# Performance work log

Measured on AMD Instinct MI355X. Metric: run time of the kernel, lower is better.

Reference implementation:

```python
import jax, jax.numpy as jnp
import numpy as np

D_MODEL = 1024
NUM_HEADS = 16
HEAD = D_MODEL // NUM_HEADS
SCALE = float(np.sqrt(D_MODEL))  # note: sqrt(d_model), as in source
LN_EPS = 1e-5


def setup_inputs() -> dict:
    key = jax.random.key(0)
    ks = jax.random.split(key, 12)
    B, Sq, Skv = 2, 2048, 2048
    s = 0.02
    return {
        "x": jax.random.normal(ks[0], (B, Sq, D_MODEL), jnp.float32),
        "enc_output": jax.random.normal(ks[1], (B, Skv, D_MODEL), jnp.float32),
        "Wq": jax.random.normal(ks[2], (D_MODEL, D_MODEL), jnp.float32) * s,
        "bq": jnp.zeros((D_MODEL,), jnp.float32),
        "Wk": jax.random.normal(ks[3], (D_MODEL, D_MODEL), jnp.float32) * s,
        "bk": jnp.zeros((D_MODEL,), jnp.float32),
        "Wv": jax.random.normal(ks[4], (D_MODEL, D_MODEL), jnp.float32) * s,
        "bv": jnp.zeros((D_MODEL,), jnp.float32),
        "Wo": jax.random.normal(ks[5], (D_MODEL, D_MODEL), jnp.float32) * s,
        "bo": jnp.zeros((D_MODEL,), jnp.float32),
        "gamma": jnp.ones((D_MODEL,), jnp.float32),
        "beta": jnp.zeros((D_MODEL,), jnp.float32),
    }


def _split_heads(t):
    B, S, _ = t.shape
    return t.reshape(B, S, NUM_HEADS, HEAD).transpose(0, 2, 1, 3)  # [B,H,S,hd]


def reference(x, enc_output, Wq, bq, Wk, bk, Wv, bv, Wo, bo, gamma, beta):
    q = _split_heads(x @ Wq.T + bq)           # [B,H,Sq,hd]
    k = _split_heads(enc_output @ Wk.T + bk)  # [B,H,Skv,hd]
    v = _split_heads(enc_output @ Wv.T + bv)  # [B,H,Skv,hd]
    scores = jnp.einsum("bhqd,bhkd->bhqk", q, k) / SCALE
    attn_weights = jax.nn.softmax(scores, axis=-1)  # dropout p=0 -> identity
    ctx = jnp.einsum("bhqk,bhkd->bhqd", attn_weights, v)
    B, H, Sq, hd = ctx.shape
    ctx = ctx.transpose(0, 2, 1, 3).reshape(B, Sq, H * hd)
    proj = ctx @ Wo.T + bo
    y = x + proj
    mu = jnp.mean(y, axis=-1, keepdims=True)
    var = jnp.var(y, axis=-1, keepdims=True)
    out = (y - mu) * jax.lax.rsqrt(var + LN_EPS) * gamma + beta
    return out, attn_weights
```

## Files before the change

### kernel.cpp

```cpp
#include <hip/hip_runtime.h>

typedef __attribute__((ext_vector_type(4))) float f32x4;
typedef __attribute__((ext_vector_type(8))) short bf16x8;
typedef __attribute__((ext_vector_type(4))) short s16x4;
typedef __attribute__((ext_vector_type(4))) unsigned u32x4;
typedef unsigned short u16;

#define GLOAD_LDS16(g, l)                                                      \
  __builtin_amdgcn_global_load_lds(                                            \
      (__attribute__((address_space(1))) const void*)(g),                      \
      (__attribute__((address_space(3))) void*)(l), 16, 0, 0)

static __device__ __forceinline__ u16 f2b(float f) {
  unsigned u = __builtin_bit_cast(unsigned, f);
  unsigned r = (u + 0x7fffu + ((u >> 16) & 1u)) >> 16;
  return (u16)r;
}

static __device__ __forceinline__ unsigned pk2(float lo, float hi) {
  unsigned r;
  asm("v_cvt_pk_bf16_f32 %0, %1, %2" : "=v"(r) : "v"(lo), "v"(hi));
  return r;
}

static __device__ __forceinline__ f32x4 mfma16(bf16x8 a, bf16x8 b, f32x4 c) {
  return __builtin_amdgcn_mfma_f32_16x16x32_bf16(a, b, c, 0, 0, 0);
}

static __device__ __forceinline__ int fsw(int row) {
  return (row & 7) ^ ((row & 8) >> 1);
}

__global__ __launch_bounds__(256) void cvt_bf16(const float* __restrict__ in,
                                                u16* __restrict__ out, int n4) {
  int i = blockIdx.x * 256 + threadIdx.x;
  int stride = gridDim.x * 256;
  for (; i < n4; i += stride) {
    float4 v = ((const float4*)in)[i];
    s16x4 o;
    o[0] = (short)f2b(v.x);
    o[1] = (short)f2b(v.y);
    o[2] = (short)f2b(v.z);
    o[3] = (short)f2b(v.w);
    ((s16x4*)out)[i] = o;
  }
}

__global__ __launch_bounds__(256) void cvt_w4(const float* __restrict__ w0,
                                              const float* __restrict__ w1,
                                              const float* __restrict__ w2,
                                              const float* __restrict__ w3,
                                              u16* __restrict__ o0,
                                              u16* __restrict__ o1,
                                              u16* __restrict__ o2,
                                              u16* __restrict__ o3) {
  int y = blockIdx.y;
  const float* in = (y == 0) ? w0 : (y == 1) ? w1 : (y == 2) ? w2 : w3;
  u16* out = (y == 0) ? o0 : (y == 1) ? o1 : (y == 2) ? o2 : o3;
  const int n4 = 262144;
  int i = blockIdx.x * 256 + threadIdx.x;
  int stride = gridDim.x * 256;
  for (; i < n4; i += stride) {
    float4 v = ((const float4*)in)[i];
    s16x4 o;
    o[0] = (short)f2b(v.x);
    o[1] = (short)f2b(v.y);
    o[2] = (short)f2b(v.z);
    o[3] = (short)f2b(v.w);
    ((s16x4*)out)[i] = o;
  }
}

#define QSCALE 0.0450842200278f
__global__ __launch_bounds__(256) void gemm_qkv3(
    const u16* __restrict__ xb, const u16* __restrict__ eb,
    const u16* __restrict__ Wqb, const u16* __restrict__ Wkb,
    const u16* __restrict__ Wvb, const float* __restrict__ bq,
    const float* __restrict__ bk, const float* __restrict__ bv,
    u16* __restrict__ Qd, u16* __restrict__ Kd, u16* __restrict__ Vtd) {
  __shared__ __align__(16) u16 As[128 * 32];
  __shared__ __align__(16) u16 Bs[128 * 32];
  const int K = 1024;
  int z = blockIdx.z;
  const u16* A = (z == 0) ? xb : eb;
  const u16* W = (z == 0) ? Wqb : (z == 1) ? Wkb : Wvb;
  const float* bias = (z == 0) ? bq : (z == 1) ? bk : bv;

  int tid = threadIdx.x;
  int w = tid >> 6, lane = tid & 63;
  int wr = w >> 1, wc = w & 1;
  int r16 = lane & 15, c4 = lane >> 4;
  int m0 = blockIdx.y * 128, n0 = blockIdx.x * 128;
  int srow = tid >> 2;
  int scol = (tid & 3) * 8;

  f32x4 acc[4][4] = {};

  const u16* ga0 = A + (size_t)(m0 + srow) * K + scol;
  const u16* gb0 = W + (size_t)(n0 + srow) * K + scol;
  char* asb = (char*)As + w * 1024;
  char* bsb = (char*)Bs + w * 1024;

  for (int k0 = 0; k0 < K; k0 += 32) {
    GLOAD_LDS16(ga0 + k0, asb);
    GLOAD_LDS16(ga0 + 64 * K + k0, asb + 4096);
    GLOAD_LDS16(gb0 + k0, bsb);
    GLOAD_LDS16(gb0 + 64 * K + k0, bsb + 4096);
    __syncthreads();
    bf16x8 af[4], bfr[4];
#pragma unroll
    for (int i = 0; i < 4; ++i)
      af[i] = *(const bf16x8*)(As + (wr * 64 + i * 16 + r16) * 32 + c4 * 8);
#pragma unroll
    for (int j = 0; j < 4; ++j)
      bfr[j] = *(const bf16x8*)(Bs + (wc * 64 + j * 16 + r16) * 32 + c4 * 8);
#pragma unroll
    for (int i = 0; i < 4; ++i)
#pragma unroll
      for (int j = 0; j < 4; ++j) acc[i][j] = mfma16(af[i], bfr[j], acc[i][j]);
    __syncthreads();
  }

  if (z < 2) {
    float oscale = (z == 0) ? QSCALE : 1.0f;
    u16* dst = (z == 0) ? Qd : Kd;
#pragma unroll
    for (int i = 0; i < 4; ++i) {
      int m = m0 + wr * 64 + i * 16 + c4 * 4;
      int b = m >> 11, s = m & 2047;
#pragma unroll
      for (int j = 0; j < 4; ++j) {
        int n = n0 + wc * 64 + j * 16 + r16;
        int h = n >> 6, d = n & 63;
        float bv = bias[n];
        u16* dp = dst + (((size_t)(b * 16 + h) * 2048 + s) * 64 + d);
#pragma unroll
        for (int r = 0; r < 4; ++r)
          dp[(size_t)r * 64] = f2b((acc[i][j][r] + bv) * oscale);
      }
    }
  } else {
#pragma unroll
    for (int i = 0; i < 4; ++i) {
      int m = m0 + wr * 64 + i * 16 + c4 * 4;
      int b = m >> 11, s = m & 2047;
#pragma unroll
      for (int j = 0; j < 4; ++j) {
        int n = n0 + wc * 64 + j * 16 + r16;
        int h = n >> 6, d = n & 63;
        float bv = bias[n];
        s16x4 o4;
#pragma unroll
        for (int r = 0; r < 4; ++r) o4[r] = (short)f2b(acc[i][j][r] + bv);
        *(s16x4*)(Vtd + ((size_t)((b * 16 + h) * 64 + d)) * 2048 + s) = o4;
      }
    }
  }
}

__global__ __launch_bounds__(256) void gemm_out(const u16* __restrict__ A,
                                                const u16* __restrict__ W,
                                                const float* __restrict__ bias,
                                                const float* __restrict__ X,
                                                float* __restrict__ Y) {
  __shared__ __align__(16) u16 As[128 * 32];
  __shared__ __align__(16) u16 Bs[128 * 32];
  const int K = 1024;
  int tid = threadIdx.x;
  int w = tid >> 6, lane = tid & 63;
  int wr = w >> 1, wc = w & 1;
  int r16 = lane & 15, c4 = lane >> 4;
  int m0 = blockIdx.y * 128, n0 = blockIdx.x * 128;
  int srow = tid >> 2;
  int scol = (tid & 3) * 8;

  f32x4 acc[4][4] = {};

  const u16* ga0 = A + (size_t)(m0 + srow) * K + scol;
  const u16* gb0 = W + (size_t)(n0 + srow) * K + scol;
  char* asb = (char*)As + w * 1024;
  char* bsb = (char*)Bs + w * 1024;

  for (int k0 = 0; k0 < K; k0 += 32) {
    GLOAD_LDS16(ga0 + k0, asb);
    GLOAD_LDS16(ga0 + 64 * K + k0, asb + 4096);
    GLOAD_LDS16(gb0 + k0, bsb);
    GLOAD_LDS16(gb0 + 64 * K + k0, bsb + 4096);
    __syncthreads();
    bf16x8 af[4], bfr[4];
#pragma unroll
    for (int i = 0; i < 4; ++i)
      af[i] = *(const bf16x8*)(As + (wr * 64 + i * 16 + r16) * 32 + c4 * 8);
#pragma unroll
    for (int j = 0; j < 4; ++j)
      bfr[j] = *(const bf16x8*)(Bs + (wc * 64 + j * 16 + r16) * 32 + c4 * 8);
#pragma unroll
    for (int i = 0; i < 4; ++i)
#pragma unroll
      for (int j = 0; j < 4; ++j) acc[i][j] = mfma16(af[i], bfr[j], acc[i][j]);
    __syncthreads();
  }

#pragma unroll
  for (int i = 0; i < 4; ++i) {
    int m = m0 + wr * 64 + i * 16 + c4 * 4;
#pragma unroll
    for (int j = 0; j < 4; ++j) {
      int n = n0 + wc * 64 + j * 16 + r16;
      float bv = bias[n];
#pragma unroll
      for (int r = 0; r < 4; ++r) {
        size_t idx = (size_t)(m + r) * 1024 + n;
        Y[idx] = acc[i][j][r] + bv + X[idx];
      }
    }
  }
}

__global__ __launch_bounds__(256, 4) void attn_k(const u16* __restrict__ Q,
                                                 const u16* __restrict__ Kg,
                                                 const u16* __restrict__ Vt,
                                                 float* __restrict__ attnw,
                                                 u16* __restrict__ ctx) {
  __shared__ __align__(16) u16 Klds[3][64 * 64];
  __shared__ __align__(16) u16 Vlds[2][64 * 64];

  int tid = threadIdx.x;
  int w = tid >> 6, lane = tid & 63;
  int r16 = lane & 15, c4 = lane >> 4;
  int id = blockIdx.x;
  int bh = id & 31, qt = id >> 5;
  int b = bh >> 4, h = bh & 15;
  int q0 = qt * 64 + w * 16;

  const u16* Qp = Q + ((size_t)bh * 2048 + q0) * 64;
  const u16* Kp = Kg + (size_t)bh * 2048 * 64;
  const u16* Vp = Vt + (size_t)bh * 64 * 2048;

  bf16x8 qf0 = *(const bf16x8*)(Qp + (size_t)r16 * 64 + c4 * 8);
  bf16x8 qf1 = *(const bf16x8*)(Qp + (size_t)r16 * 64 + 32 + c4 * 8);

  int perm0 = ((r16 >> 2) << 3) + (r16 & 3);
  int srow0 = w * 8 + (lane >> 3);
  int sc = lane & 7;

#define STAGE_K(bufi, kv)                                                      \
  {                                                                            \
    _Pragma("unroll") for (int i = 0; i < 2; ++i) {                            \
      int row = i * 32 + srow0;                                                \
      int ch = sc ^ fsw(row);                                                  \
      GLOAD_LDS16(Kp + (size_t)(((kv) & 2047) + row) * 64 + ch * 8,            \
                  (u16*)&Klds[bufi][0] + w * 512 + i * 2048);                  \
    }                                                                          \
  }
#define STAGE_V(bufi, kv)                                                      \
  {                                                                            \
    _Pragma("unroll") for (int i = 0; i < 2; ++i) {                            \
      int row = i * 32 + srow0;                                                \
      int ch = sc ^ fsw(row);                                                  \
      GLOAD_LDS16(Vp + (size_t)row * 2048 + ((kv) & 2047) + ch * 8,            \
                  (u16*)&Vlds[bufi][0] + w * 512 + i * 2048);                  \
    }                                                                          \
  }
#define LDSF(base, row, chunk)                                                 \
  (*(const bf16x8*)((base) + (row) * 64 + (((chunk) ^ fsw(row)) << 3)))
#define WAIT_BAR(n)                                                            \
  {                                                                            \
    asm volatile("s_waitcnt vmcnt(" #n ")" ::: "memory");                      \
    __builtin_amdgcn_s_barrier();                                              \
  }

  float sum = 0.f;
  STAGE_K(0, 0);
  STAGE_K(1, 64);
  WAIT_BAR(2);
  {
    int wbuf = 2, rbuf = 0;
    for (int kv0 = 0; kv0 < 2048; kv0 += 64) {
      STAGE_K(wbuf, kv0 + 128);
      const u16* Kb = &Klds[rbuf][0];
#pragma unroll
      for (int s = 0; s < 2; ++s) {
        int ra = s * 32 + perm0;
        bf16x8 k00 = LDSF(Kb, ra, c4);
        bf16x8 k01 = LDSF(Kb, ra, c4 + 4);
        bf16x8 k10 = LDSF(Kb, ra + 4, c4);
        bf16x8 k11 = LDSF(Kb, ra + 4, c4 + 4);
        f32x4 s0 = {}, s1 = {};
        __builtin_amdgcn_s_setprio(1);
        s0 = mfma16(k00, qf0, s0);
        s0 = mfma16(k01, qf1, s0);
        s1 = mfma16(k10, qf0, s1);
        s1 = mfma16(k11, qf1, s1);
        __builtin_amdgcn_s_setprio(0);
#pragma unroll
        for (int r = 0; r < 4; ++r)
          sum += __builtin_amdgcn_exp2f(s0[r]) + __builtin_amdgcn_exp2f(s1[r]);
      }
      WAIT_BAR(2);
      wbuf = (wbuf == 2) ? 0 : wbuf + 1;
      rbuf = (rbuf == 2) ? 0 : rbuf + 1;
    }
  }
  sum += __shfl_xor(sum, 16, 64);
  sum += __shfl_xor(sum, 32, 64);
  float nls = -__log2f(sum);

  asm volatile("s_waitcnt vmcnt(0)" ::: "memory");
  __builtin_amdgcn_s_barrier();

  f32x4 o[4] = {};
  float* ap = attnw + ((size_t)bh * 2048 + q0 + r16) * 2048;
  STAGE_V(0, 0);
  STAGE_K(0, 0);
  STAGE_K(1, 64);
  WAIT_BAR(2);
  {
    int wbuf = 2, rbuf = 0;
    int t = 0;
    for (int kv0 = 0; kv0 < 2048; kv0 += 64, ++t) {
      STAGE_V((t + 1) & 1, kv0 + 64);
      STAGE_K(wbuf, kv0 + 128);
      const u16* Kb = &Klds[rbuf][0];
      const u16* Vb = &Vlds[t & 1][0];
#pragma unroll
      for (int s = 0; s < 2; ++s) {
        int ra = s * 32 + perm0;
        bf16x8 k00 = LDSF(Kb, ra, c4);
        bf16x8 k01 = LDSF(Kb, ra, c4 + 4);
        bf16x8 k10 = LDSF(Kb, ra + 4, c4);
        bf16x8 k11 = LDSF(Kb, ra + 4, c4 + 4);
        f32x4 s0 = {}, s1 = {};
        __builtin_amdgcn_s_setprio(1);
        s0 = mfma16(k00, qf0, s0);
        s0 = mfma16(k01, qf1, s0);
        s1 = mfma16(k10, qf0, s1);
        s1 = mfma16(k11, qf1, s1);
        __builtin_amdgcn_s_setprio(0);
        f32x4 p0, p1;
#pragma unroll
        for (int r = 0; r < 4; ++r) {
          p0[r] = __builtin_amdgcn_exp2f(s0[r] + nls);
          p1[r] = __builtin_amdgcn_exp2f(s1[r] + nls);
        }
        u32x4 pk;
        pk[0] = pk2(p0[0], p0[1]);
        pk[1] = pk2(p0[2], p0[3]);
        pk[2] = pk2(p1[0], p1[1]);
        pk[3] = pk2(p1[2], p1[3]);
        bf16x8 pf = __builtin_bit_cast(bf16x8, pk);
        bf16x8 v0 = LDSF(Vb, 0 * 16 + r16, s * 4 + c4);
        bf16x8 v1 = LDSF(Vb, 1 * 16 + r16, s * 4 + c4);
        bf16x8 v2 = LDSF(Vb, 2 * 16 + r16, s * 4 + c4);
        bf16x8 v3 = LDSF(Vb, 3 * 16 + r16, s * 4 + c4);
        __builtin_amdgcn_s_setprio(1);
        o[0] = mfma16(pf, v0, o[0]);
        o[1] = mfma16(pf, v1, o[1]);
        o[2] = mfma16(pf, v2, o[2]);
        o[3] = mfma16(pf, v3, o[3]);
        __builtin_amdgcn_s_setprio(0);
        int kvc = kv0 + s * 32 + c4 * 8;
        *(f32x4*)(ap + kvc) = p0;
        *(f32x4*)(ap + kvc + 4) = p1;
      }
      WAIT_BAR(6);
      wbuf = (wbuf == 2) ? 0 : wbuf + 1;
      rbuf = (rbuf == 2) ? 0 : rbuf + 1;
    }
  }

#pragma unroll
  for (int dt = 0; dt < 4; ++dt)
#pragma unroll
    for (int r = 0; r < 4; ++r)
      ctx[((size_t)(b * 2048 + q0 + c4 * 4 + r)) * 1024 + h * 64 + dt * 16 +
          r16] = f2b(o[dt][r]);
#undef STAGE_K
#undef STAGE_V
#undef LDSF
#undef WAIT_BAR
}

__global__ __launch_bounds__(256) void ln_k(const float* __restrict__ Y,
                                            const float* __restrict__ gamma,
                                            const float* __restrict__ beta,
                                            float* __restrict__ out) {
  int row = blockIdx.x * 4 + (threadIdx.x >> 6);
  int lane = threadIdx.x & 63;
  const float* yr = Y + (size_t)row * 1024;
  float4 v[4];
  float sum = 0.f, sq = 0.f;
#pragma unroll
  for (int i = 0; i < 4; ++i) {
    v[i] = *(const float4*)(yr + i * 256 + lane * 4);
    sum += v[i].x + v[i].y + v[i].z + v[i].w;
    sq += v[i].x * v[i].x + v[i].y * v[i].y + v[i].z * v[i].z + v[i].w * v[i].w;
  }
#pragma unroll
  for (int m = 1; m < 64; m <<= 1) {
    sum += __shfl_xor(sum, m, 64);
    sq += __shfl_xor(sq, m, 64);
  }
  float mu = sum * (1.f / 1024.f);
  float var = sq * (1.f / 1024.f) - mu * mu;
  float rs = rsqrtf(var + 1e-5f);
  float* orow = out + (size_t)row * 1024;
#pragma unroll
  for (int i = 0; i < 4; ++i) {
    int c = i * 256 + lane * 4;
    float4 g = *(const float4*)(gamma + c);
    float4 be = *(const float4*)(beta + c);
    float4 o;
    o.x = (v[i].x - mu) * rs * g.x + be.x;
    o.y = (v[i].y - mu) * rs * g.y + be.y;
    o.z = (v[i].z - mu) * rs * g.z + be.z;
    o.w = (v[i].w - mu) * rs * g.w + be.w;
    *(float4*)(orow + c) = o;
  }
}

extern "C" void kernel_launch(void* const* d_in, const int* in_sizes, int n_in,
                              void* d_out, int out_size, void* d_ws,
                              size_t ws_size, hipStream_t stream) {
  const float* x = (const float*)d_in[0];
  const float* enc = (const float*)d_in[1];
  const float* Wq = (const float*)d_in[2];
  const float* bq = (const float*)d_in[3];
  const float* Wk = (const float*)d_in[4];
  const float* bk = (const float*)d_in[5];
  const float* Wv = (const float*)d_in[6];
  const float* bv = (const float*)d_in[7];
  const float* Wo = (const float*)d_in[8];
  const float* bo = (const float*)d_in[9];
  const float* gamma = (const float*)d_in[10];
  const float* beta = (const float*)d_in[11];

  float* out = (float*)d_out;
  float* attnw = out + (size_t)4194304;

  char* ws = (char*)d_ws;
  u16* xb = (u16*)(ws + (size_t)0);
  u16* eb = (u16*)(ws + ((size_t)8 << 20));
  u16* Wqb = (u16*)(ws + ((size_t)16 << 20));
  u16* Wkb = (u16*)(ws + ((size_t)18 << 20));
  u16* Wvb = (u16*)(ws + ((size_t)20 << 20));
  u16* Wob = (u16*)(ws + ((size_t)22 << 20));
  u16* Qws = (u16*)(ws + ((size_t)24 << 20));
  u16* Kws = (u16*)(ws + ((size_t)32 << 20));
  u16* Vt = (u16*)(ws + ((size_t)48 << 20));
  u16* ctx = (u16*)(ws + ((size_t)40 << 20));
  float* Yws = (float*)(ws + (size_t)0);

  cvt_bf16<<<dim3(1024), 256, 0, stream>>>(x, xb, 1048576);
  cvt_bf16<<<dim3(1024), 256, 0, stream>>>(enc, eb, 1048576);
  cvt_w4<<<dim3(256, 4), 256, 0, stream>>>(Wq, Wk, Wv, Wo, Wqb, Wkb, Wvb, Wob);

  gemm_qkv3<<<dim3(8, 32, 3), 256, 0, stream>>>(xb, eb, Wqb, Wkb, Wvb, bq, bk,
                                                bv, Qws, Kws, Vt);

  attn_k<<<dim3(1024), 256, 0, stream>>>(Qws, Kws, Vt, attnw, ctx);

  gemm_out<<<dim3(8, 32), 256, 0, stream>>>(ctx, Wob, bo, x, Yws);

  ln_k<<<dim3(1024), 256, 0, stream>>>(Yws, gamma, beta, out);
}
```

Measured before the change: 294.2 us.

## Split softmax row-sum pass into separate kernel with doubled query rows per warp

Moves the first attention pass (exp-sum over all keys to get the log-normalizer) into its own kernel, where each warp handles 32 query rows instead of 16, so every K fragment loaded from LDS feeds twice as many MFMAs. The normalizers are written to a workspace buffer and read back by the second kernel, which computes the probabilities, writes the attention weights and accumulates PV. This halves the K staging traffic and block count for the sum pass. The cost is an extra launch, a small global round trip for the normalizers, and higher register use in the sum kernel.

```diff
diff --git a/kernel.cpp b/kernel.cpp
--- a/kernel.cpp
+++ b/kernel.cpp
@@ -217,28 +217,28 @@
   }
 }
 
-__global__ __launch_bounds__(256, 4) void attn_k(const u16* __restrict__ Q,
-                                                 const u16* __restrict__ Kg,
-                                                 const u16* __restrict__ Vt,
-                                                 float* __restrict__ attnw,
-                                                 u16* __restrict__ ctx) {
+__global__ __launch_bounds__(256, 4) void sum_k(const u16* __restrict__ Q,
+                                                const u16* __restrict__ Kg,
+                                                float* __restrict__ nlsbuf) {
   __shared__ __align__(16) u16 Klds[3][64 * 64];
-  __shared__ __align__(16) u16 Vlds[2][64 * 64];
 
   int tid = threadIdx.x;
   int w = tid >> 6, lane = tid & 63;
   int r16 = lane & 15, c4 = lane >> 4;
   int id = blockIdx.x;
   int bh = id & 31, qt = id >> 5;
-  int b = bh >> 4, h = bh & 15;
-  int q0 = qt * 64 + w * 16;
+  int q0 = qt * 128 + w * 32;
 
   const u16* Qp = Q + ((size_t)bh * 2048 + q0) * 64;
   const u16* Kp = Kg + (size_t)bh * 2048 * 64;
-  const u16* Vp = Vt + (size_t)bh * 64 * 2048;
-
-  bf16x8 qf0 = *(const bf16x8*)(Qp + (size_t)r16 * 64 + c4 * 8);
-  bf16x8 qf1 = *(const bf16x8*)(Qp + (size_t)r16 * 64 + 32 + c4 * 8);
+
+  bf16x8 qf[2][2];
+#pragma unroll
+  for (int hh = 0; hh < 2; ++hh)
+#pragma unroll
+    for (int ch = 0; ch < 2; ++ch)
+      qf[hh][ch] = *(const bf16x8*)(Qp + (size_t)(hh * 16 + r16) * 64 +
+                                    ch * 32 + c4 * 8);
 
   int perm0 = ((r16 >> 2) << 3) + (r16 & 3);
   int srow0 = w * 8 + (lane >> 3);
@@ -253,6 +253,105 @@
                   (u16*)&Klds[bufi][0] + w * 512 + i * 2048);                  \
     }                                                                          \
   }
+#define LDSF(base, row, chunk)                                                 \
+  (*(const bf16x8*)((base) + (row) * 64 + (((chunk) ^ fsw(row)) << 3)))
+#define WAIT_BAR(n)                                                            \
+  {                                                                            \
+    asm volatile("s_waitcnt vmcnt(" #n ")" ::: "memory");                      \
+    __builtin_amdgcn_s_barrier();                                              \
+  }
+
+  float sumA = 0.f, sumB = 0.f;
+  STAGE_K(0, 0);
+  STAGE_K(1, 64);
+  WAIT_BAR(2);
+  {
+    int wbuf = 2, rbuf = 0;
+    for (int kv0 = 0; kv0 < 2048; kv0 += 64) {
+      STAGE_K(wbuf, kv0 + 128);
+      const u16* Kb = &Klds[rbuf][0];
+#pragma unroll
+      for (int s = 0; s < 2; ++s) {
+        int ra = s * 32 + perm0;
+        bf16x8 k00 = LDSF(Kb, ra, c4);
+        bf16x8 k01 = LDSF(Kb, ra, c4 + 4);
+        bf16x8 k10 = LDSF(Kb, ra + 4, c4);
+        bf16x8 k11 = LDSF(Kb, ra + 4, c4 + 4);
+        f32x4 s0A = {}, s1A = {}, s0B = {}, s1B = {};
+        __builtin_amdgcn_s_setprio(1);
+        s0A = mfma16(k00, qf[0][0], s0A);
+        s0A = mfma16(k01, qf[0][1], s0A);
+        s1A = mfma16(k10, qf[0][0], s1A);
+        s1A = mfma16(k11, qf[0][1], s1A);
+        s0B = mfma16(k00, qf[1][0], s0B);
+        s0B = mfma16(k01, qf[1][1], s0B);
+        s1B = mfma16(k10, qf[1][0], s1B);
+        s1B = mfma16(k11, qf[1][1], s1B);
+        __builtin_amdgcn_s_setprio(0);
+#pragma unroll
+        for (int r = 0; r < 4; ++r) {
+          sumA +=
+              __builtin_amdgcn_exp2f(s0A[r]) + __builtin_amdgcn_exp2f(s1A[r]);
+          sumB +=
+              __builtin_amdgcn_exp2f(s0B[r]) + __builtin_amdgcn_exp2f(s1B[r]);
+        }
+      }
+      WAIT_BAR(2);
+      wbuf = (wbuf == 2) ? 0 : wbuf + 1;
+      rbuf = (rbuf == 2) ? 0 : rbuf + 1;
+    }
+  }
+  sumA += __shfl_xor(sumA, 16, 64);
+  sumA += __shfl_xor(sumA, 32, 64);
+  sumB += __shfl_xor(sumB, 16, 64);
+  sumB += __shfl_xor(sumB, 32, 64);
+  if (c4 == 0) {
+    nlsbuf[(size_t)bh * 2048 + q0 + r16] = -__log2f(sumA);
+    nlsbuf[(size_t)bh * 2048 + q0 + 16 + r16] = -__log2f(sumB);
+  }
+#undef STAGE_K
+#undef LDSF
+#undef WAIT_BAR
+}
+
+__global__ __launch_bounds__(256, 4) void attn_pv(const u16* __restrict__ Q,
+                                                  const u16* __restrict__ Kg,
+                                                  const u16* __restrict__ Vt,
+                                                  const float* __restrict__ nlsbuf,
+                                                  float* __restrict__ attnw,
+                                                  u16* __restrict__ ctx) {
+  __shared__ __align__(16) u16 Klds[3][64 * 64];
+  __shared__ __align__(16) u16 Vlds[2][64 * 64];
+
+  int tid = threadIdx.x;
+  int w = tid >> 6, lane = tid & 63;
+  int r16 = lane & 15, c4 = lane >> 4;
+  int id = blockIdx.x;
+  int bh = id & 31, qt = id >> 5;
+  int b = bh >> 4, h = bh & 15;
+  int q0 = qt * 64 + w * 16;
+
+  const u16* Qp = Q + ((size_t)bh * 2048 + q0) * 64;
+  const u16* Kp = Kg + (size_t)bh * 2048 * 64;
+  const u16* Vp = Vt + (size_t)bh * 64 * 2048;
+
+  bf16x8 qf0 = *(const bf16x8*)(Qp + (size_t)r16 * 64 + c4 * 8);
+  bf16x8 qf1 = *(const bf16x8*)(Qp + (size_t)r16 * 64 + 32 + c4 * 8);
+  float nls = nlsbuf[(size_t)bh * 2048 + q0 + r16];
+
+  int perm0 = ((r16 >> 2) << 3) + (r16 & 3);
+  int srow0 = w * 8 + (lane >> 3);
+  int sc = lane & 7;
+
+#define STAGE_K(bufi, kv)                                                      \
+  {                                                                            \
+    _Pragma("unroll") for (int i = 0; i < 2; ++i) {                            \
+      int row = i * 32 + srow0;                                                \
+      int ch = sc ^ fsw(row);                                                  \
+      GLOAD_LDS16(Kp + (size_t)(((kv) & 2047) + row) * 64 + ch * 8,            \
+                  (u16*)&Klds[bufi][0] + w * 512 + i * 2048);                  \
+    }                                                                          \
+  }
 #define STAGE_V(bufi, kv)                                                      \
   {                                                                            \
     _Pragma("unroll") for (int i = 0; i < 2; ++i) {                            \
@@ -269,45 +368,6 @@
     asm volatile("s_waitcnt vmcnt(" #n ")" ::: "memory");                      \
     __builtin_amdgcn_s_barrier();                                              \
   }
-
-  float sum = 0.f;
-  STAGE_K(0, 0);
-  STAGE_K(1, 64);
-  WAIT_BAR(2);
-  {
-    int wbuf = 2, rbuf = 0;
-    for (int kv0 = 0; kv0 < 2048; kv0 += 64) {
-      STAGE_K(wbuf, kv0 + 128);
-      const u16* Kb = &Klds[rbuf][0];
-#pragma unroll
-      for (int s = 0; s < 2; ++s) {
-        int ra = s * 32 + perm0;
-        bf16x8 k00 = LDSF(Kb, ra, c4);
-        bf16x8 k01 = LDSF(Kb, ra, c4 + 4);
-        bf16x8 k10 = LDSF(Kb, ra + 4, c4);
-        bf16x8 k11 = LDSF(Kb, ra + 4, c4 + 4);
-        f32x4 s0 = {}, s1 = {};
-        __builtin_amdgcn_s_setprio(1);
-        s0 = mfma16(k00, qf0, s0);
-        s0 = mfma16(k01, qf1, s0);
-        s1 = mfma16(k10, qf0, s1);
-        s1 = mfma16(k11, qf1, s1);
-        __builtin_amdgcn_s_setprio(0);
-#pragma unroll
-        for (int r = 0; r < 4; ++r)
-          sum += __builtin_amdgcn_exp2f(s0[r]) + __builtin_amdgcn_exp2f(s1[r]);
-      }
-      WAIT_BAR(2);
-      wbuf = (wbuf == 2) ? 0 : wbuf + 1;
-      rbuf = (rbuf == 2) ? 0 : rbuf + 1;
-    }
-  }
-  sum += __shfl_xor(sum, 16, 64);
-  sum += __shfl_xor(sum, 32, 64);
-  float nls = -__log2f(sum);
-
-  asm volatile("s_waitcnt vmcnt(0)" ::: "memory");
-  __builtin_amdgcn_s_barrier();
 
   f32x4 o[4] = {};
   float* ap = attnw + ((size_t)bh * 2048 + q0 + r16) * 2048;
@@ -449,6 +509,7 @@
   u16* Kws = (u16*)(ws + ((size_t)32 << 20));
   u16* Vt = (u16*)(ws + ((size_t)48 << 20));
   u16* ctx = (u16*)(ws + ((size_t)40 << 20));
+  float* nlsbuf = (float*)(ws + ((size_t)56 << 20));
   float* Yws = (float*)(ws + (size_t)0);
 
   cvt_bf16<<<dim3(1024), 256, 0, stream>>>(x, xb, 1048576);
@@ -458,7 +519,8 @@
   gemm_qkv3<<<dim3(8, 32, 3), 256, 0, stream>>>(xb, eb, Wqb, Wkb, Wvb, bq, bk,
                                                 bv, Qws, Kws, Vt);
 
-  attn_k<<<dim3(1024), 256, 0, stream>>>(Qws, Kws, Vt, attnw, ctx);
+  sum_k<<<dim3(512), 256, 0, stream>>>(Qws, Kws, nlsbuf);
+  attn_pv<<<dim3(1024), 256, 0, stream>>>(Qws, Kws, Vt, nlsbuf, attnw, ctx);
 
   gemm_out<<<dim3(8, 32), 256, 0, stream>>>(ctx, Wob, bo, x, Yws);
 
```

After: 309.2 us. +5.1%, slower.

## Split attention KV range across two wave groups per block

Applied to the files above, without the earlier changes.

Doubles the attention block to 512 threads. Two groups of four waves each process half of the 2048-long KV sequence for the same 64 query rows, with separate LDS staging buffers. The softmax denominators are combined through a small LDS reduction, and the partial context outputs are summed through LDS before being written. This halves the serial KV loop per wave to expose more parallelism and memory-level concurrency, at the cost of doubled LDS per block, extra barriers and a reduction step.

```diff
diff --git a/kernel.cpp b/kernel.cpp
--- a/kernel.cpp
+++ b/kernel.cpp
@@ -217,21 +217,23 @@
   }
 }
 
-__global__ __launch_bounds__(256, 4) void attn_k(const u16* __restrict__ Q,
+__global__ __launch_bounds__(512, 4) void attn_k(const u16* __restrict__ Q,
                                                  const u16* __restrict__ Kg,
                                                  const u16* __restrict__ Vt,
                                                  float* __restrict__ attnw,
                                                  u16* __restrict__ ctx) {
-  __shared__ __align__(16) u16 Klds[3][64 * 64];
-  __shared__ __align__(16) u16 Vlds[2][64 * 64];
+  __shared__ __align__(16) u16 Klds[2][3][64 * 64];
+  __shared__ __align__(16) u16 Vlds[2][2][64 * 64];
 
   int tid = threadIdx.x;
   int w = tid >> 6, lane = tid & 63;
+  int g = w >> 2, wq = w & 3;
   int r16 = lane & 15, c4 = lane >> 4;
   int id = blockIdx.x;
   int bh = id & 31, qt = id >> 5;
   int b = bh >> 4, h = bh & 15;
-  int q0 = qt * 64 + w * 16;
+  int q0 = qt * 64 + wq * 16;
+  int kvB = g << 10;
 
   const u16* Qp = Q + ((size_t)bh * 2048 + q0) * 64;
   const u16* Kp = Kg + (size_t)bh * 2048 * 64;
@@ -241,7 +243,7 @@
   bf16x8 qf1 = *(const bf16x8*)(Qp + (size_t)r16 * 64 + 32 + c4 * 8);
 
   int perm0 = ((r16 >> 2) << 3) + (r16 & 3);
-  int srow0 = w * 8 + (lane >> 3);
+  int srow0 = wq * 8 + (lane >> 3);
   int sc = lane & 7;
 
 #define STAGE_K(bufi, kv)                                                      \
@@ -249,8 +251,8 @@
     _Pragma("unroll") for (int i = 0; i < 2; ++i) {                            \
       int row = i * 32 + srow0;                                                \
       int ch = sc ^ fsw(row);                                                  \
-      GLOAD_LDS16(Kp + (size_t)(((kv) & 2047) + row) * 64 + ch * 8,            \
-                  (u16*)&Klds[bufi][0] + w * 512 + i * 2048);                  \
+      GLOAD_LDS16(Kp + (size_t)(kvB + ((kv) & 1023) + row) * 64 + ch * 8,      \
+                  (u16*)&Klds[g][bufi][0] + wq * 512 + i * 2048);              \
     }                                                                          \
   }
 #define STAGE_V(bufi, kv)                                                      \
@@ -258,8 +260,8 @@
     _Pragma("unroll") for (int i = 0; i < 2; ++i) {                            \
       int row = i * 32 + srow0;                                                \
       int ch = sc ^ fsw(row);                                                  \
-      GLOAD_LDS16(Vp + (size_t)row * 2048 + ((kv) & 2047) + ch * 8,            \
-                  (u16*)&Vlds[bufi][0] + w * 512 + i * 2048);                  \
+      GLOAD_LDS16(Vp + (size_t)row * 2048 + kvB + ((kv) & 1023) + ch * 8,      \
+                  (u16*)&Vlds[g][bufi][0] + wq * 512 + i * 2048);              \
     }                                                                          \
   }
 #define LDSF(base, row, chunk)                                                 \
@@ -276,9 +278,9 @@
   WAIT_BAR(2);
   {
     int wbuf = 2, rbuf = 0;
-    for (int kv0 = 0; kv0 < 2048; kv0 += 64) {
+    for (int kv0 = 0; kv0 < 1024; kv0 += 64) {
       STAGE_K(wbuf, kv0 + 128);
-      const u16* Kb = &Klds[rbuf][0];
+      const u16* Kb = &Klds[g][rbuf][0];
 #pragma unroll
       for (int s = 0; s < 2; ++s) {
         int ra = s * 32 + perm0;
@@ -304,13 +306,17 @@
   }
   sum += __shfl_xor(sum, 16, 64);
   sum += __shfl_xor(sum, 32, 64);
-  float nls = -__log2f(sum);
-
-  asm volatile("s_waitcnt vmcnt(0)" ::: "memory");
-  __builtin_amdgcn_s_barrier();
+
+  float* redbuf = (float*)&Vlds[0][0][0];
+  __syncthreads();
+  if (lane < 16) redbuf[(g * 4 + wq) * 16 + lane] = sum;
+  __syncthreads();
+  float stot = redbuf[(0 * 4 + wq) * 16 + r16] + redbuf[(1 * 4 + wq) * 16 + r16];
+  float nls = -__log2f(stot);
+  __syncthreads();
 
   f32x4 o[4] = {};
-  float* ap = attnw + ((size_t)bh * 2048 + q0 + r16) * 2048;
+  float* ap = attnw + ((size_t)bh * 2048 + q0 + r16) * 2048 + kvB;
   STAGE_V(0, 0);
   STAGE_K(0, 0);
   STAGE_K(1, 64);
@@ -318,11 +324,11 @@
   {
     int wbuf = 2, rbuf = 0;
     int t = 0;
-    for (int kv0 = 0; kv0 < 2048; kv0 += 64, ++t) {
+    for (int kv0 = 0; kv0 < 1024; kv0 += 64, ++t) {
       STAGE_V((t + 1) & 1, kv0 + 64);
       STAGE_K(wbuf, kv0 + 128);
-      const u16* Kb = &Klds[rbuf][0];
-      const u16* Vb = &Vlds[t & 1][0];
+      const u16* Kb = &Klds[g][rbuf][0];
+      const u16* Vb = &Vlds[g][t & 1][0];
 #pragma unroll
       for (int s = 0; s < 2; ++s) {
         int ra = s * 32 + perm0;
@@ -369,12 +375,24 @@
     }
   }
 
-#pragma unroll
-  for (int dt = 0; dt < 4; ++dt)
-#pragma unroll
-    for (int r = 0; r < 4; ++r)
-      ctx[((size_t)(b * 2048 + q0 + c4 * 4 + r)) * 1024 + h * 64 + dt * 16 +
-          r16] = f2b(o[dt][r]);
+  __syncthreads();
+  float* cbuf = (float*)&Klds[0][0][0];
+  if (g == 1) {
+#pragma unroll
+    for (int dt = 0; dt < 4; ++dt)
+      *(f32x4*)&cbuf[(wq * 64 + lane) * 16 + dt * 4] = o[dt];
+  }
+  __syncthreads();
+  if (g == 0) {
+#pragma unroll
+    for (int dt = 0; dt < 4; ++dt) {
+      f32x4 o1 = *(const f32x4*)&cbuf[(wq * 64 + lane) * 16 + dt * 4];
+#pragma unroll
+      for (int r = 0; r < 4; ++r)
+        ctx[((size_t)(b * 2048 + q0 + c4 * 4 + r)) * 1024 + h * 64 + dt * 16 +
+            r16] = f2b(o[dt][r] + o1[r]);
+    }
+  }
 #undef STAGE_K
 #undef STAGE_V
 #undef LDSF
@@ -458,7 +476,7 @@
   gemm_qkv3<<<dim3(8, 32, 3), 256, 0, stream>>>(xb, eb, Wqb, Wkb, Wvb, bq, bk,
                                                 bv, Qws, Kws, Vt);
 
-  attn_k<<<dim3(1024), 256, 0, stream>>>(Qws, Kws, Vt, attnw, ctx);
+  attn_k<<<dim3(1024), 512, 0, stream>>>(Qws, Kws, Vt, attnw, ctx);
 
   gemm_out<<<dim3(8, 32), 256, 0, stream>>>(ctx, Wob, bo, x, Yws);
 
```

Result: faster. 259.9 us (-11.7%).
